# Optimization experiments

Measured on AMD Instinct MI355X. Metric: run time of the kernel, lower is better.

The kernel has to match this reference:

```python
import jax, jax.numpy as jnp
import numpy as np

B, L, H, D = 2, 2048, 8, 64
LOCAL_WINDOW = 32   # init arg
STRIDE = 64         # init arg


def _sparse_mask(L_Q, L_K, dtype):
    # Self-attention branch (L_Q == L_K): union of a local band of half-width
    # local_window//2 and strided diagonals at offsets that are multiples of (stride+1).
    i = jnp.arange(L_Q)[:, None]
    j = jnp.arange(L_K)[None, :]
    d = jnp.abs(i - j)
    band = d <= (LOCAL_WINDOW // 2)
    strided = (d % (STRIDE + 1)) == 0
    return (band | strided).astype(dtype)


def setup_inputs() -> dict:
    key = jax.random.key(0)
    kx, kq, kk, kv = jax.random.split(key, 4)
    x = jax.random.normal(kx, (B, L, H, D), jnp.float32)
    queries = jax.random.normal(kq, (B, L, H, D), jnp.float32)
    keys = jax.random.normal(kk, (B, L, H, D), jnp.float32)
    values = jax.random.normal(kv, (B, L, H, D), jnp.float32)
    # TriangularCausalMask: True on strictly upper triangle -> masked with -inf
    causal = jnp.triu(jnp.ones((L, L), dtype=bool), k=1)
    attn_mask = jnp.broadcast_to(causal[None, None], (B, 1, L, L))
    return {"x": x, "queries": queries, "keys": keys, "values": values,
            "attn_mask": attn_mask}


def reference(x, queries, keys, values, attn_mask):
    Bq, L_Q, Hh, Dh = queries.shape
    L_K = keys.shape[1]
    scale = 1.0 / np.sqrt(Dh)  # self.scale is None
    # [B,H,L_Q,L_K]
    scores = jnp.einsum('blhe,bshe->bhls', queries, keys)
    sparse = _sparse_mask(L_Q, L_K, scores.dtype)  # [L_Q, L_K]
    # NOTE: torch code ZEROES (not -inf) the non-sparse entries, then applies
    # the causal mask with -inf, then softmaxes scale*scores. Faithful here.
    scores = scores * sparse
    scores = jnp.where(attn_mask, -jnp.inf, scores)
    A = jax.nn.softmax(scale * scores, axis=-1)  # dropout = identity (eval)
    V = jnp.einsum('bhls,bshd->blhd', A, values)
    return V
```

## Files before the change

### kernel.cpp

```cpp
#include <hip/hip_runtime.h>

#define Bc 2
#define Lc 2048
#define Hc 8
#define Dc 64
#define TL 16
#define NT (Lc / TL)
#define RHD (Hc * Dc)
#define SP1 65
#define SCALE 0.125f

template <int CTRL>
__device__ __forceinline__ float dpp_add(float x) {
    int p = __builtin_amdgcn_update_dpp(0, __float_as_int(x), CTRL, 0xF, 0xF, true);
    return x + __int_as_float(p);
}
__device__ __forceinline__ float row16_sum(float x) {
    x = dpp_add<0xB1>(x);
    x = dpp_add<0x4E>(x);
    x = dpp_add<0x141>(x);
    x = dpp_add<0x140>(x);
    return x;
}

__global__ __launch_bounds__(256)
void dozer_chunk_sum(const float* __restrict__ V, float* __restrict__ partials) {
    const int bh = blockIdx.x;
    const int t  = blockIdx.y;
    const int b  = bh >> 3;
    const int h  = bh & 7;
    const int g  = threadIdx.x >> 6;
    const int d  = threadIdx.x & 63;
    const float* Vbh = V + (size_t)b * Lc * RHD + h * Dc;
    const int l0 = t * TL;
    float s = 0.f;
    for (int r = g; r < TL; r += 4)
        s += Vbh[(size_t)(l0 + r) * RHD + d];
    __shared__ float red[4][64];
    red[g][d] = s;
    __syncthreads();
    if (g == 0)
        partials[((size_t)bh * NT + t) * 64 + d] =
            red[0][d] + red[1][d] + red[2][d] + red[3][d];
}

__global__ __launch_bounds__(256)
void dozer_main(const float* __restrict__ Q, const float* __restrict__ K,
                const float* __restrict__ V, const float* __restrict__ partials,
                float* __restrict__ out) {
    const int bh   = blockIdx.x;
    const int t    = (NT - 1) - blockIdx.y;
    const int b    = bh >> 3;
    const int h    = bh & 7;
    const int tid  = threadIdx.x;
    const int wave = tid >> 6;
    const int lane = tid & 63;
    const int l0   = t * TL;

    const float* Qbh = Q + (size_t)b * Lc * RHD + h * Dc;
    const float* Kbh = K + (size_t)b * Lc * RHD + h * Dc;
    const float* Vbh = V + (size_t)b * Lc * RHD + h * Dc;

    __shared__ float Kband[32][64];
    __shared__ float Vband[32][64];
    __shared__ float Ptile[TL][64];
    float (*red)[64] = (float(*)[64])Kband;

    {
        const int d = lane;
        float pbase = 0.f;
        if (partials) {
            const float* pb = partials + (size_t)bh * NT * 64;
            #pragma unroll 4
            for (int c = wave; c < t; c += 4)
                pbase += pb[(size_t)c * 64 + d];
        } else {
            for (int s = wave; s < l0; s += 4)
                pbase += Vbh[(size_t)s * RHD + d];
        }
        const float* vr = Vbh + (size_t)(l0 + 4 * wave) * RHD + d;
        const float x0 = vr[0];
        const float x1 = vr[RHD];
        const float x2 = vr[2 * RHD];
        const float x3 = vr[3 * RHD];
        const float s0 = x0, s1 = s0 + x1, s2 = s1 + x2, s3 = s2 + x3;
        red[wave][d]     = pbase;
        red[4 + wave][d] = s3;
        __syncthreads();
        float base = red[0][d] + red[1][d] + red[2][d] + red[3][d];
        if (wave > 0) base += red[4][d];
        if (wave > 1) base += red[5][d];
        if (wave > 2) base += red[6][d];
        Ptile[4 * wave + 0][d] = base + s0;
        Ptile[4 * wave + 1][d] = base + s1;
        Ptile[4 * wave + 2][d] = base + s2;
        Ptile[4 * wave + 3][d] = base + s3;
        __syncthreads();
    }

    {
        const int i  = tid >> 4;
        const int c4 = (tid & 15) * 4;
        #pragma unroll
        for (int rnd = 0; rnd < 2; ++rnd) {
            const int ii = i + 16 * rnd;
            int j = l0 - 16 + ii; if (j < 0) j = 0;
            *(float4*)&Kband[ii][c4] = *(const float4*)(Kbh + (size_t)j * RHD + c4);
            *(float4*)&Vband[ii][c4] = *(const float4*)(Vbh + (size_t)j * RHD + c4);
        }
        __syncthreads();
    }

    const int p  = lane >> 4;
    const int dd = lane & 15;

    for (int rr = 0; rr < 4; ++rr) {
        const int r = wave * 4 + rr;
        const int l = l0 + r;
        const int nk   = l / SP1;
        const int nfar = (nk + 3) >> 2;

        float4 q4 = *(const float4*)&Qbh[(size_t)l * RHD + dd * 4];
        q4.x *= SCALE; q4.y *= SCALE; q4.z *= SCALE; q4.w *= SCALE;

        float4 acc = make_float4(0.f, 0.f, 0.f, 0.f);
        float  den = 0.f;

        auto farload = [&](float4& k4, float4& v4, int m) {
            const int f = 1 + p + 4 * m;
            int j = l - SP1 * f; if (j < 0) j = 0;
            k4 = *(const float4*)(Kbh + (size_t)j * RHD + dd * 4);
            v4 = *(const float4*)(Vbh + (size_t)j * RHD + dd * 4);
        };
        auto farstep = [&](const float4& k4, const float4& v4, int m) {
            const int f = 1 + p + 4 * m;
            const bool ok = (f <= nk);
            float dot = q4.x * k4.x + q4.y * k4.y + q4.z * k4.z + q4.w * k4.w;
            dot = row16_sum(dot);
            float w = __expf(dot) - 1.f;
            w = ok ? w : 0.f;
            acc.x += w * v4.x; acc.y += w * v4.y;
            acc.z += w * v4.z; acc.w += w * v4.w;
            den += w;
        };

        float4 kA = make_float4(0.f,0.f,0.f,0.f), vA = kA, kB = kA, vB = kA;
        if (nfar > 0) farload(kA, vA, 0);
        if (nfar > 1) farload(kB, vB, 1);

        #pragma unroll
        for (int it = 0; it < 4; ++it) {
            const int off = p + 4 * it;
            const int idx = r + 16 - off;
            const bool ok = (off <= l);
            const float4 k4 = *(const float4*)&Kband[idx][dd * 4];
            const float4 v4 = *(const float4*)&Vband[idx][dd * 4];
            float dot = q4.x * k4.x + q4.y * k4.y + q4.z * k4.z + q4.w * k4.w;
            dot = row16_sum(dot);
            float w = __expf(dot) - 1.f;
            w = ok ? w : 0.f;
            acc.x += w * v4.x; acc.y += w * v4.y;
            acc.z += w * v4.z; acc.w += w * v4.w;
            den += w;
        }
        {
            const bool ok = (p == 0) && (l >= 16);
            const float4 k4 = *(const float4*)&Kband[r][dd * 4];
            const float4 v4 = *(const float4*)&Vband[r][dd * 4];
            float dot = q4.x * k4.x + q4.y * k4.y + q4.z * k4.z + q4.w * k4.w;
            dot = row16_sum(dot);
            float w = __expf(dot) - 1.f;
            w = ok ? w : 0.f;
            acc.x += w * v4.x; acc.y += w * v4.y;
            acc.z += w * v4.z; acc.w += w * v4.w;
            den += w;
        }

        int m = 0;
        for (; m + 1 < nfar; m += 2) {
            farstep(kA, vA, m);
            if (m + 2 < nfar) farload(kA, vA, m + 2);
            farstep(kB, vB, m + 1);
            if (m + 3 < nfar) farload(kB, vB, m + 3);
        }
        if (m < nfar) farstep(kA, vA, m);

        acc.x += __shfl_xor(acc.x, 16, 64); acc.x += __shfl_xor(acc.x, 32, 64);
        acc.y += __shfl_xor(acc.y, 16, 64); acc.y += __shfl_xor(acc.y, 32, 64);
        acc.z += __shfl_xor(acc.z, 16, 64); acc.z += __shfl_xor(acc.z, 32, 64);
        acc.w += __shfl_xor(acc.w, 16, 64); acc.w += __shfl_xor(acc.w, 32, 64);
        den   += __shfl_xor(den, 16, 64);   den   += __shfl_xor(den, 32, 64);

        const float inv = 1.f / ((float)(l + 1) + den);
        if (p == 0) {
            const float4 P4 = *(const float4*)&Ptile[r][dd * 4];
            float4 o;
            o.x = (P4.x + acc.x) * inv;
            o.y = (P4.y + acc.y) * inv;
            o.z = (P4.z + acc.z) * inv;
            o.w = (P4.w + acc.w) * inv;
            *(float4*)&out[((size_t)(b * Lc + l) * Hc + h) * Dc + dd * 4] = o;
        }
    }
}

extern "C" void kernel_launch(void* const* d_in, const int* in_sizes, int n_in,
                              void* d_out, int out_size, void* d_ws, size_t ws_size,
                              hipStream_t stream) {
    const float* Q = (const float*)d_in[1];
    const float* K = (const float*)d_in[2];
    const float* V = (const float*)d_in[3];
    float* out = (float*)d_out;

    const size_t need = (size_t)Bc * Hc * NT * 64 * sizeof(float);
    float* partials = (ws_size >= need) ? (float*)d_ws : nullptr;

    dim3 grid(Bc * Hc, NT);
    if (partials)
        dozer_chunk_sum<<<grid, 256, 0, stream>>>(V, partials);
    dozer_main<<<grid, 256, 0, stream>>>(Q, K, V, partials, out);
}
```

Measured before the change: 118.7 us.

## Split strided far-diagonal attention into a residue-class kernel with shared K/V reuse

Adds a dozer_far kernel that groups query rows by residue modulo 65. Each block loads that class's K/V rows (at most 32) into shared memory once, and each thread pair handles a short and a long row so the triangular work is balanced. The far contributions go to workspace buffers that a lighter main kernel adds on top of the local band. The main kernel also reduces chunk partials with float4 loads across all lanes and uses padded shared arrays. This removes the repeated scattered global loads of far K/V per row, at the cost of an extra launch and a workspace round trip for the far accumulators.

```diff
diff --git a/kernel.cpp b/kernel.cpp
--- a/kernel.cpp
+++ b/kernel.cpp
@@ -45,6 +45,221 @@
 }
 
 __global__ __launch_bounds__(256)
+void dozer_far(const float* __restrict__ Q, const float* __restrict__ K,
+               const float* __restrict__ V, float* __restrict__ facc,
+               float* __restrict__ fden) {
+    const int bh   = blockIdx.x;
+    const int c    = blockIdx.y;
+    const int b    = bh >> 3;
+    const int h    = bh & 7;
+    const int tid  = threadIdx.x;
+    const int wave = tid >> 6;
+    const int lane = tid & 63;
+    const int p    = lane >> 4;
+    const int dd   = lane & 15;
+    const int n    = (Lc - 1 - c) / SP1 + 1;
+
+    const float* Qbh = Q + (size_t)b * Lc * RHD + h * Dc;
+    const float* Kbh = K + (size_t)b * Lc * RHD + h * Dc;
+    const float* Vbh = V + (size_t)b * Lc * RHD + h * Dc;
+
+    __shared__ float Kc[32][64];
+    __shared__ float Vc[32][64];
+
+    {
+        const int ri = tid >> 4;
+        const int c4 = (tid & 15) * 4;
+        #pragma unroll
+        for (int rnd = 0; rnd < 2; ++rnd) {
+            const int k = ri + 16 * rnd;
+            if (k < n) {
+                const size_t row = (size_t)(c + SP1 * k) * RHD;
+                *(float4*)&Kc[k][c4] = *(const float4*)(Kbh + row + c4);
+                *(float4*)&Vc[k][c4] = *(const float4*)(Vbh + row + c4);
+            }
+        }
+        __syncthreads();
+    }
+
+    const int s  = wave + 4 * p;
+    const int i1 = s;
+    const int i2 = n - 1 - s;
+    const int l1 = c + SP1 * i1;
+    const int l2 = c + SP1 * i2;
+
+    float4 q1 = *(const float4*)&Qbh[(size_t)l1 * RHD + dd * 4];
+    float4 q2 = *(const float4*)&Qbh[(size_t)l2 * RHD + dd * 4];
+    q1.x *= SCALE; q1.y *= SCALE; q1.z *= SCALE; q1.w *= SCALE;
+    q2.x *= SCALE; q2.y *= SCALE; q2.z *= SCALE; q2.w *= SCALE;
+
+    float4 a1 = make_float4(0.f, 0.f, 0.f, 0.f);
+    float4 a2 = make_float4(0.f, 0.f, 0.f, 0.f);
+    float  d1 = 0.f, d2 = 0.f;
+
+    for (int j = 0; j < i2; ++j) {
+        const float4 k4 = *(const float4*)&Kc[j][dd * 4];
+        const float4 v4 = *(const float4*)&Vc[j][dd * 4];
+        float t2 = q2.x * k4.x + q2.y * k4.y + q2.z * k4.z + q2.w * k4.w;
+        t2 = row16_sum(t2);
+        const float w2 = __expf(t2) - 1.f;
+        a2.x += w2 * v4.x; a2.y += w2 * v4.y;
+        a2.z += w2 * v4.z; a2.w += w2 * v4.w;
+        d2 += w2;
+        float t1 = q1.x * k4.x + q1.y * k4.y + q1.z * k4.z + q1.w * k4.w;
+        t1 = row16_sum(t1);
+        float w1 = __expf(t1) - 1.f;
+        w1 = (j < i1) ? w1 : 0.f;
+        a1.x += w1 * v4.x; a1.y += w1 * v4.y;
+        a1.z += w1 * v4.z; a1.w += w1 * v4.w;
+        d1 += w1;
+    }
+
+    {
+        float* f2 = facc + ((size_t)bh * Lc + l2) * 64 + dd * 4;
+        *(float4*)f2 = a2;
+        if (dd == 0) fden[(size_t)bh * Lc + l2] = d2;
+        if (i1 != i2) {
+            float* f1 = facc + ((size_t)bh * Lc + l1) * 64 + dd * 4;
+            *(float4*)f1 = a1;
+            if (dd == 0) fden[(size_t)bh * Lc + l1] = d1;
+        }
+    }
+}
+
+__global__ __launch_bounds__(256)
+void dozer_main_lite(const float* __restrict__ Q, const float* __restrict__ K,
+                     const float* __restrict__ V, const float* __restrict__ partials,
+                     const float* __restrict__ facc, const float* __restrict__ fden,
+                     float* __restrict__ out) {
+    const int bh   = blockIdx.x;
+    const int t    = (NT - 1) - blockIdx.y;
+    const int b    = bh >> 3;
+    const int h    = bh & 7;
+    const int tid  = threadIdx.x;
+    const int wave = tid >> 6;
+    const int lane = tid & 63;
+    const int l0   = t * TL;
+    const int p    = lane >> 4;
+    const int dd   = lane & 15;
+
+    const float* Qbh = Q + (size_t)b * Lc * RHD + h * Dc;
+    const float* Kbh = K + (size_t)b * Lc * RHD + h * Dc;
+    const float* Vbh = V + (size_t)b * Lc * RHD + h * Dc;
+
+    __shared__ float Kband[32][68];
+    __shared__ float Vband[32][68];
+    __shared__ float Ptile[TL][64];
+    float* redf = &Kband[0][0];
+
+    {
+        float4 pa = make_float4(0.f, 0.f, 0.f, 0.f);
+        const float* pb = partials + (size_t)bh * NT * 64;
+        const int itn = (t + 15) >> 4;
+        for (int it = 0; it < itn; ++it) {
+            const int cc = 16 * it + 4 * wave + p;
+            const float4 f4 = *(const float4*)(pb + (size_t)cc * 64 + dd * 4);
+            if (cc < t) { pa.x += f4.x; pa.y += f4.y; pa.z += f4.z; pa.w += f4.w; }
+        }
+        *(float4*)&redf[(4 * wave + p) * 68 + dd * 4] = pa;
+
+        const int d = lane;
+        const float* vr = Vbh + (size_t)(l0 + 4 * wave) * RHD + d;
+        const float x0 = vr[0];
+        const float x1 = vr[RHD];
+        const float x2 = vr[2 * RHD];
+        const float x3 = vr[3 * RHD];
+        const float s0 = x0, s1 = s0 + x1, s2 = s1 + x2, s3 = s2 + x3;
+        redf[(16 + wave) * 68 + d] = s3;
+        __syncthreads();
+        float base = 0.f;
+        #pragma unroll
+        for (int r2 = 0; r2 < 16; ++r2) base += redf[r2 * 68 + d];
+        if (wave > 0) base += redf[(16 + 0) * 68 + d];
+        if (wave > 1) base += redf[(16 + 1) * 68 + d];
+        if (wave > 2) base += redf[(16 + 2) * 68 + d];
+        Ptile[4 * wave + 0][d] = base + s0;
+        Ptile[4 * wave + 1][d] = base + s1;
+        Ptile[4 * wave + 2][d] = base + s2;
+        Ptile[4 * wave + 3][d] = base + s3;
+        __syncthreads();
+    }
+
+    {
+        const int i  = tid >> 4;
+        const int c4 = (tid & 15) * 4;
+        #pragma unroll
+        for (int rnd = 0; rnd < 2; ++rnd) {
+            const int ii = i + 16 * rnd;
+            int j = l0 - 16 + ii; if (j < 0) j = 0;
+            *(float4*)&Kband[ii][c4] = *(const float4*)(Kbh + (size_t)j * RHD + c4);
+            *(float4*)&Vband[ii][c4] = *(const float4*)(Vbh + (size_t)j * RHD + c4);
+        }
+        __syncthreads();
+    }
+
+    for (int rr = 0; rr < 4; ++rr) {
+        const int r = wave * 4 + rr;
+        const int l = l0 + r;
+
+        float4 q4 = *(const float4*)&Qbh[(size_t)l * RHD + dd * 4];
+        q4.x *= SCALE; q4.y *= SCALE; q4.z *= SCALE; q4.w *= SCALE;
+
+        float4 acc = make_float4(0.f, 0.f, 0.f, 0.f);
+        float  den = 0.f;
+
+        #pragma unroll
+        for (int it = 0; it < 4; ++it) {
+            const int off = p + 4 * it;
+            const int idx = r + 16 - off;
+            const bool ok = (off <= l);
+            const float4 k4 = *(const float4*)&Kband[idx][dd * 4];
+            const float4 v4 = *(const float4*)&Vband[idx][dd * 4];
+            float dot = q4.x * k4.x + q4.y * k4.y + q4.z * k4.z + q4.w * k4.w;
+            dot = row16_sum(dot);
+            float w = __expf(dot) - 1.f;
+            w = ok ? w : 0.f;
+            acc.x += w * v4.x; acc.y += w * v4.y;
+            acc.z += w * v4.z; acc.w += w * v4.w;
+            den += w;
+        }
+        {
+            const bool ok = (p == 0) && (l >= 16);
+            const float4 k4 = *(const float4*)&Kband[r][dd * 4];
+            const float4 v4 = *(const float4*)&Vband[r][dd * 4];
+            float dot = q4.x * k4.x + q4.y * k4.y + q4.z * k4.z + q4.w * k4.w;
+            dot = row16_sum(dot);
+            float w = __expf(dot) - 1.f;
+            w = ok ? w : 0.f;
+            acc.x += w * v4.x; acc.y += w * v4.y;
+            acc.z += w * v4.z; acc.w += w * v4.w;
+            den += w;
+        }
+
+        acc.x += __shfl_xor(acc.x, 16, 64); acc.x += __shfl_xor(acc.x, 32, 64);
+        acc.y += __shfl_xor(acc.y, 16, 64); acc.y += __shfl_xor(acc.y, 32, 64);
+        acc.z += __shfl_xor(acc.z, 16, 64); acc.z += __shfl_xor(acc.z, 32, 64);
+        acc.w += __shfl_xor(acc.w, 16, 64); acc.w += __shfl_xor(acc.w, 32, 64);
+        den   += __shfl_xor(den, 16, 64);   den   += __shfl_xor(den, 32, 64);
+
+        if (p == 0) {
+            const size_t rowix = (size_t)bh * Lc + l;
+            const float4 f4 = *(const float4*)(facc + rowix * 64 + dd * 4);
+            const float  fd = fden[rowix];
+            acc.x += f4.x; acc.y += f4.y; acc.z += f4.z; acc.w += f4.w;
+            den   += fd;
+            const float inv = 1.f / ((float)(l + 1) + den);
+            const float4 P4 = *(const float4*)&Ptile[r][dd * 4];
+            float4 o;
+            o.x = (P4.x + acc.x) * inv;
+            o.y = (P4.y + acc.y) * inv;
+            o.z = (P4.z + acc.z) * inv;
+            o.w = (P4.w + acc.w) * inv;
+            *(float4*)&out[((size_t)(b * Lc + l) * Hc + h) * Dc + dd * 4] = o;
+        }
+    }
+}
+
+__global__ __launch_bounds__(256)
 void dozer_main(const float* __restrict__ Q, const float* __restrict__ K,
                 const float* __restrict__ V, const float* __restrict__ partials,
                 float* __restrict__ out) {
@@ -212,11 +427,23 @@
     const float* V = (const float*)d_in[3];
     float* out = (float*)d_out;
 
-    const size_t need = (size_t)Bc * Hc * NT * 64 * sizeof(float);
-    float* partials = (ws_size >= need) ? (float*)d_ws : nullptr;
+    const size_t np = (size_t)Bc * Hc * NT * 64 * sizeof(float);
+    const size_t nf = (size_t)Bc * Hc * Lc * 64 * sizeof(float);
+    const size_t nd = (size_t)Bc * Hc * Lc * sizeof(float);
 
     dim3 grid(Bc * Hc, NT);
-    if (partials)
+    if (ws_size >= np + nf + nd && d_ws != nullptr) {
+        char* ws = (char*)d_ws;
+        float* partials = (float*)ws;
+        float* facc     = (float*)(ws + np);
+        float* fden     = (float*)(ws + np + nf);
         dozer_chunk_sum<<<grid, 256, 0, stream>>>(V, partials);
-    dozer_main<<<grid, 256, 0, stream>>>(Q, K, V, partials, out);
-}
+        dozer_far<<<dim3(Bc * Hc, SP1), 256, 0, stream>>>(Q, K, V, facc, fden);
+        dozer_main_lite<<<grid, 256, 0, stream>>>(Q, K, V, partials, facc, fden, out);
+    } else {
+        float* partials = (ws_size >= np && d_ws != nullptr) ? (float*)d_ws : nullptr;
+        if (partials)
+            dozer_chunk_sum<<<grid, 256, 0, stream>>>(V, partials);
+        dozer_main<<<grid, 256, 0, stream>>>(Q, K, V, partials, out);
+    }
+}
```

Measured after the change: 124.5 us. +4.9%, slower.

## Hoist band loads, vectorize prefix partial sums, deepen far-key prefetch to four

Applied to the files above, without the earlier changes.

Issues the K/V band global loads at kernel start so they overlap the prefix-sum phase, and stores them to shared memory afterward. The partial-chunk reduction now uses float4 loads spread over 16 lane groups, with fixed unrolled loads guarded by t, instead of a strided scalar loop. The strided far-key loop keeps four K/V pairs in flight instead of two, and launch bounds request four blocks per CU. The cost is higher register pressure from the extra prefetch buffers and hoisted loads, which could limit occupancy or cause spills.

```diff
diff --git a/kernel.cpp b/kernel.cpp
--- a/kernel.cpp
+++ b/kernel.cpp
@@ -44,7 +44,7 @@
             red[0][d] + red[1][d] + red[2][d] + red[3][d];
 }
 
-__global__ __launch_bounds__(256)
+__global__ __launch_bounds__(256, 4)
 void dozer_main(const float* __restrict__ Q, const float* __restrict__ K,
                 const float* __restrict__ V, const float* __restrict__ partials,
                 float* __restrict__ out) {
@@ -56,6 +56,8 @@
     const int wave = tid >> 6;
     const int lane = tid & 63;
     const int l0   = t * TL;
+    const int p    = lane >> 4;
+    const int dd   = lane & 15;
 
     const float* Qbh = Q + (size_t)b * Lc * RHD + h * Dc;
     const float* Kbh = K + (size_t)b * Lc * RHD + h * Dc;
@@ -64,33 +66,65 @@
     __shared__ float Kband[32][64];
     __shared__ float Vband[32][64];
     __shared__ float Ptile[TL][64];
-    float (*red)[64] = (float(*)[64])Kband;
+    float* redf = &Kband[0][0];
+
+    const int si = tid >> 4;
+    const int c4 = (tid & 15) * 4;
+    int jb0 = l0 - 16 + si; if (jb0 < 0) jb0 = 0;
+    const int jb1 = l0 + si;
+    const float4 kS0 = *(const float4*)(Kbh + (size_t)jb0 * RHD + c4);
+    const float4 vS0 = *(const float4*)(Vbh + (size_t)jb0 * RHD + c4);
+    const float4 kS1 = *(const float4*)(Kbh + (size_t)jb1 * RHD + c4);
+    const float4 vS1 = *(const float4*)(Vbh + (size_t)jb1 * RHD + c4);
 
     {
+        const int cc0 = 4 * wave + p;
+        float4 pa = make_float4(0.f, 0.f, 0.f, 0.f);
+        if (partials) {
+            const float* pb = partials + (size_t)bh * NT * 64 + dd * 4;
+            if (t > 0) {
+                const float4 f0 = *(const float4*)(pb + (size_t)(cc0     ) * 64);
+                const float4 f1 = *(const float4*)(pb + (size_t)(cc0 + 16) * 64);
+                const float4 f2 = *(const float4*)(pb + (size_t)(cc0 + 32) * 64);
+                const float4 f3 = *(const float4*)(pb + (size_t)(cc0 + 48) * 64);
+                if (cc0      < t) { pa.x += f0.x; pa.y += f0.y; pa.z += f0.z; pa.w += f0.w; }
+                if (cc0 + 16 < t) { pa.x += f1.x; pa.y += f1.y; pa.z += f1.z; pa.w += f1.w; }
+                if (cc0 + 32 < t) { pa.x += f2.x; pa.y += f2.y; pa.z += f2.z; pa.w += f2.w; }
+                if (cc0 + 48 < t) { pa.x += f3.x; pa.y += f3.y; pa.z += f3.z; pa.w += f3.w; }
+            }
+            if (t > 64) {
+                const float4 f4 = *(const float4*)(pb + (size_t)(cc0 +  64) * 64);
+                const float4 f5 = *(const float4*)(pb + (size_t)(cc0 +  80) * 64);
+                const float4 f6 = *(const float4*)(pb + (size_t)(cc0 +  96) * 64);
+                const float4 f7 = *(const float4*)(pb + (size_t)(cc0 + 112) * 64);
+                if (cc0 +  64 < t) { pa.x += f4.x; pa.y += f4.y; pa.z += f4.z; pa.w += f4.w; }
+                if (cc0 +  80 < t) { pa.x += f5.x; pa.y += f5.y; pa.z += f5.z; pa.w += f5.w; }
+                if (cc0 +  96 < t) { pa.x += f6.x; pa.y += f6.y; pa.z += f6.z; pa.w += f6.w; }
+                if (cc0 + 112 < t) { pa.x += f7.x; pa.y += f7.y; pa.z += f7.z; pa.w += f7.w; }
+            }
+        } else {
+            for (int s = cc0; s < l0; s += 16) {
+                const float4 v4 = *(const float4*)(Vbh + (size_t)s * RHD + dd * 4);
+                pa.x += v4.x; pa.y += v4.y; pa.z += v4.z; pa.w += v4.w;
+            }
+        }
+        *(float4*)&redf[cc0 * 64 + dd * 4] = pa;
+
         const int d = lane;
-        float pbase = 0.f;
-        if (partials) {
-            const float* pb = partials + (size_t)bh * NT * 64;
-            #pragma unroll 4
-            for (int c = wave; c < t; c += 4)
-                pbase += pb[(size_t)c * 64 + d];
-        } else {
-            for (int s = wave; s < l0; s += 4)
-                pbase += Vbh[(size_t)s * RHD + d];
-        }
         const float* vr = Vbh + (size_t)(l0 + 4 * wave) * RHD + d;
         const float x0 = vr[0];
         const float x1 = vr[RHD];
         const float x2 = vr[2 * RHD];
         const float x3 = vr[3 * RHD];
         const float s0 = x0, s1 = s0 + x1, s2 = s1 + x2, s3 = s2 + x3;
-        red[wave][d]     = pbase;
-        red[4 + wave][d] = s3;
+        redf[(16 + wave) * 64 + d] = s3;
         __syncthreads();
-        float base = red[0][d] + red[1][d] + red[2][d] + red[3][d];
-        if (wave > 0) base += red[4][d];
-        if (wave > 1) base += red[5][d];
-        if (wave > 2) base += red[6][d];
+        float base = 0.f;
+        #pragma unroll
+        for (int r2 = 0; r2 < 16; ++r2) base += redf[r2 * 64 + d];
+        if (wave > 0) base += redf[16 * 64 + d];
+        if (wave > 1) base += redf[17 * 64 + d];
+        if (wave > 2) base += redf[18 * 64 + d];
         Ptile[4 * wave + 0][d] = base + s0;
         Ptile[4 * wave + 1][d] = base + s1;
         Ptile[4 * wave + 2][d] = base + s2;
@@ -98,21 +132,11 @@
         __syncthreads();
     }
 
-    {
-        const int i  = tid >> 4;
-        const int c4 = (tid & 15) * 4;
-        #pragma unroll
-        for (int rnd = 0; rnd < 2; ++rnd) {
-            const int ii = i + 16 * rnd;
-            int j = l0 - 16 + ii; if (j < 0) j = 0;
-            *(float4*)&Kband[ii][c4] = *(const float4*)(Kbh + (size_t)j * RHD + c4);
-            *(float4*)&Vband[ii][c4] = *(const float4*)(Vbh + (size_t)j * RHD + c4);
-        }
-        __syncthreads();
-    }
-
-    const int p  = lane >> 4;
-    const int dd = lane & 15;
+    *(float4*)&Kband[si][c4]      = kS0;
+    *(float4*)&Vband[si][c4]      = vS0;
+    *(float4*)&Kband[si + 16][c4] = kS1;
+    *(float4*)&Vband[si + 16][c4] = vS1;
+    __syncthreads();
 
     for (int rr = 0; rr < 4; ++rr) {
         const int r = wave * 4 + rr;
@@ -144,9 +168,11 @@
             den += w;
         };
 
-        float4 kA = make_float4(0.f,0.f,0.f,0.f), vA = kA, kB = kA, vB = kA;
-        if (nfar > 0) farload(kA, vA, 0);
-        if (nfar > 1) farload(kB, vB, 1);
+        float4 k0, v0, k1, v1, k2, v2, k3, v3;
+        if (nfar > 0) farload(k0, v0, 0);
+        if (nfar > 1) farload(k1, v1, 1);
+        if (nfar > 2) farload(k2, v2, 2);
+        if (nfar > 3) farload(k3, v3, 3);
 
         #pragma unroll
         for (int it = 0; it < 4; ++it) {
@@ -177,13 +203,15 @@
         }
 
         int m = 0;
-        for (; m + 1 < nfar; m += 2) {
-            farstep(kA, vA, m);
-            if (m + 2 < nfar) farload(kA, vA, m + 2);
-            farstep(kB, vB, m + 1);
-            if (m + 3 < nfar) farload(kB, vB, m + 3);
-        }
-        if (m < nfar) farstep(kA, vA, m);
+        for (; m + 4 <= nfar; m += 4) {
+            farstep(k0, v0, m    ); if (m + 4 < nfar) farload(k0, v0, m + 4);
+            farstep(k1, v1, m + 1); if (m + 5 < nfar) farload(k1, v1, m + 5);
+            farstep(k2, v2, m + 2); if (m + 6 < nfar) farload(k2, v2, m + 6);
+            farstep(k3, v3, m + 3); if (m + 7 < nfar) farload(k3, v3, m + 7);
+        }
+        if (m     < nfar) farstep(k0, v0, m);
+        if (m + 1 < nfar) farstep(k1, v1, m + 1);
+        if (m + 2 < nfar) farstep(k2, v2, m + 2);
 
         acc.x += __shfl_xor(acc.x, 16, 64); acc.x += __shfl_xor(acc.x, 32, 64);
         acc.y += __shfl_xor(acc.y, 16, 64); acc.y += __shfl_xor(acc.y, 32, 64);
@@ -212,8 +240,8 @@
     const float* V = (const float*)d_in[3];
     float* out = (float*)d_out;
 
-    const size_t need = (size_t)Bc * Hc * NT * 64 * sizeof(float);
-    float* partials = (ws_size >= need) ? (float*)d_ws : nullptr;
+    const size_t np = (size_t)Bc * Hc * NT * 64 * sizeof(float);
+    float* partials = (ws_size >= np && d_ws != nullptr) ? (float*)d_ws : nullptr;
 
     dim3 grid(Bc * Hc, NT);
     if (partials)
```

Measured after the change: 121.8 us. 2.6% more time.
